# Kernel optimization log

Measured on AMD Instinct MI355X. Metric: run time of the kernel, lower is better.

Reference implementation:

```python
import jax, jax.numpy as jnp
import numpy as np

NEG_SLOPE = 0.01


def reference(feat_src, feat_dst, src, dst, attn_l, attn_r):
    # feat_src: [Ns, D], feat_dst: [Nd, D], src/dst: [E] int, attn_*: [1, D]
    n_dst = feat_dst.shape[0]
    el = (feat_src * attn_l).sum(axis=-1)  # [Ns]
    er = (feat_dst * attn_r).sum(axis=-1)  # [Nd]
    e = el[src] + er[dst]                  # [E]
    e = jnp.where(e >= 0, e, NEG_SLOPE * e)  # leaky_relu
    # edge softmax over incoming edges of each destination node
    m = jax.ops.segment_max(e, dst, num_segments=n_dst)  # [Nd]
    m = jnp.where(jnp.isfinite(m), m, 0.0)  # guard empty segments
    a = jnp.exp(e - m[dst])                 # [E]
    denom = jax.ops.segment_sum(a, dst, num_segments=n_dst)  # [Nd]
    denom = jnp.where(denom > 0, denom, 1.0)
    a = a / denom[dst]
    # weighted scatter-sum of source features: [E, D] messages -> [Nd, D]
    msg = feat_src[src] * a[:, None]
    out = jax.ops.segment_sum(msg, dst, num_segments=n_dst)
    return out


def setup_inputs() -> dict:
    key = jax.random.key(0)
    k1, k2, k3, k4, k5, k6 = jax.random.split(key, 6)
    Ns, Nd, E, D = 100000, 100000, 1600000, 128
    return {
        "feat_src": jax.random.normal(k1, (Ns, D), dtype=jnp.float32),
        "feat_dst": jax.random.normal(k2, (Nd, D), dtype=jnp.float32),
        "src": jax.random.randint(k3, (E,), 0, Ns, dtype=jnp.int32),
        "dst": jax.random.randint(k4, (E,), 0, Nd, dtype=jnp.int32),
        "attn_l": jax.random.normal(k5, (1, D), dtype=jnp.float32) * 0.1,
        "attn_r": jax.random.normal(k6, (1, D), dtype=jnp.float32) * 0.1,
    }
```

## Files before the change

### kernel.cpp

```cpp
#include <hip/hip_runtime.h>
#include <hip/hip_bf16.h>
#include <math.h>

#define D 128
#define AGG_THREADS 128
#define CHUNK 512
#define BSHIFT 8
#define MAXB 512
#define MAXWG 1024
#define PCHUNK 2048
#define PE 8
#define EBUF_CAP 5120
#define PR 8192

__device__ __forceinline__ unsigned short f2bf(float f) {
    union { float f; unsigned int u; } c; c.f = f;
    unsigned int u = c.u;
    unsigned int r = (u + 0x7FFFu + ((u >> 16) & 1u)) >> 16;
    return (unsigned short)r;
}
__device__ __forceinline__ void unpack2(unsigned int w, float& lo, float& hi) {
    union { unsigned int u; float f; } c;
    c.u = w << 16;          lo = c.f;
    c.u = w & 0xFFFF0000u;  hi = c.f;
}

__device__ __forceinline__ int scan8w(const int* __restrict__ arr, int* __restrict__ outp,
                                      int n, int tid, int* wsum8) {
    int wv = tid >> 6, lane = tid & 63;
    int nchunk = (n + 63) >> 6;
    int cpw = (nchunk + 7) >> 3;
    int c0 = wv * cpw, c1 = min(nchunk, c0 + cpw);
    int carry = 0;
    for (int c = c0; c < c1; ++c) {
        int i = (c << 6) + lane;
        int v = (i < n) ? arr[i] : 0;
        int x = v;
        #pragma unroll
        for (int off = 1; off < 64; off <<= 1) {
            int t = __shfl_up(x, off, 64);
            if (lane >= off) x += t;
        }
        if (i < n) outp[i] = x - v + carry;
        carry += __shfl(x, 63, 64);
    }
    if (lane == 0) wsum8[wv] = carry;
    __syncthreads();
    int wbase = 0;
    for (int u = 0; u < wv; ++u) wbase += wsum8[u];
    if (wbase) {
        for (int c = c0; c < c1; ++c) {
            int i = (c << 6) + lane;
            if (i < n) outp[i] += wbase;
        }
    }
    int tot = 0;
    #pragma unroll
    for (int u = 0; u < 8; ++u) tot += wsum8[u];
    __syncthreads();
    return tot;
}

__global__ void prep_partition_kernel(const float* __restrict__ feat_src,
                                      const float* __restrict__ feat_dst,
                                      const float* __restrict__ attn_l,
                                      const float* __restrict__ attn_r,
                                      float* __restrict__ el, float* __restrict__ er,
                                      unsigned short* __restrict__ feat_bf,
                                      int Ns, int Nd,
                                      const int* __restrict__ src,
                                      const int* __restrict__ dst,
                                      int E, int nbk, int nwg,
                                      uint2* __restrict__ bins,
                                      int* __restrict__ cnt_tab,
                                      int* __restrict__ loc_tab) {
    __shared__ int hist[MAXB];
    __shared__ int lstart[MAXB];
    __shared__ int cursor[MAXB];
    __shared__ uint2 sbuf[PCHUNK];
    int tid = threadIdx.x;

    if ((int)blockIdx.x < nwg) {
        int w = blockIdx.x;
        int e0 = w * PCHUNK;
        int e1 = min(E, e0 + PCHUNK);
        int n = e1 - e0;

        for (int i = tid; i < nbk; i += 256) hist[i] = 0;
        __syncthreads();

        int es[PE], ed[PE];
        #pragma unroll
        for (int k = 0; k < PE; ++k) {
            int idx = e0 + k * 256 + tid;
            if (idx < e1) {
                es[k] = src[idx];
                ed[k] = dst[idx];
                atomicAdd(&hist[ed[k] >> BSHIFT], 1);
            }
        }
        __syncthreads();

        if (tid < 64) {
            int carry = 0;
            for (int c = 0; c < nbk; c += 64) {
                int i = c + tid;
                int v = (i < nbk) ? hist[i] : 0;
                int x = v;
                #pragma unroll
                for (int off = 1; off < 64; off <<= 1) {
                    int t = __shfl_up(x, off, 64);
                    if (tid >= off) x += t;
                }
                if (i < nbk) lstart[i] = x - v + carry;
                carry += __shfl(x, 63, 64);
            }
        }
        __syncthreads();

        for (int i = tid; i < nbk; i += 256) {
            cnt_tab[(size_t)w * nbk + i] = hist[i];
            loc_tab[(size_t)w * nbk + i] = lstart[i];
            cursor[i] = 0;
        }
        __syncthreads();

        #pragma unroll
        for (int k = 0; k < PE; ++k) {
            int idx = e0 + k * 256 + tid;
            if (idx < e1) {
                int b = ed[k] >> BSHIFT;
                int r = lstart[b] + atomicAdd(&cursor[b], 1);
                sbuf[r] = make_uint2((unsigned)es[k], (unsigned)ed[k]);
            }
        }
        __syncthreads();

        uint2* obase = bins + (size_t)w * PCHUNK;
        for (int t = tid; t < n; t += 256) obase[t] = sbuf[t];
    } else {
        int half = tid >> 5;
        int lane = tid & 31;
        int node = ((int)blockIdx.x - nwg) * 8 + half;
        if (node >= Ns + Nd) return;
        bool is_src = node < Ns;
        const float* feat = is_src ? feat_src + (size_t)node * D
                                   : feat_dst + (size_t)(node - Ns) * D;
        const float* attn = is_src ? attn_l : attn_r;
        float4 a = ((const float4*)attn)[lane];
        float4 v = ((const float4*)feat)[lane];
        if (is_src) {
            ushort4 h; h.x = f2bf(v.x); h.y = f2bf(v.y); h.z = f2bf(v.z); h.w = f2bf(v.w);
            ((ushort4*)(feat_bf + (size_t)node * D))[lane] = h;
        }
        float s = v.x * a.x + v.y * a.y + v.z * a.z + v.w * a.w;
        #pragma unroll
        for (int off = 16; off > 0; off >>= 1)
            s += __shfl_xor(s, off, 64);
        if (lane == 0) {
            if (is_src) el[node] = s;
            else        er[node - Ns] = s;
        }
    }
}

__global__ void prep_kernel(const float* __restrict__ feat_src,
                            const float* __restrict__ feat_dst,
                            const float* __restrict__ attn_l,
                            const float* __restrict__ attn_r,
                            float* __restrict__ el, float* __restrict__ er,
                            unsigned short* __restrict__ feat_bf, int store_bf,
                            int Ns, int Nd) {
    int half = threadIdx.x >> 5;
    int lane = threadIdx.x & 31;
    int node = blockIdx.x * 8 + half;
    if (node >= Ns + Nd) return;
    bool is_src = node < Ns;
    const float* feat = is_src ? feat_src + (size_t)node * D
                               : feat_dst + (size_t)(node - Ns) * D;
    const float* attn = is_src ? attn_l : attn_r;
    float4 a = ((const float4*)attn)[lane];
    float4 v = ((const float4*)feat)[lane];
    if (is_src && store_bf) {
        ushort4 h; h.x = f2bf(v.x); h.y = f2bf(v.y); h.z = f2bf(v.z); h.w = f2bf(v.w);
        ((ushort4*)(feat_bf + (size_t)node * D))[lane] = h;
    }
    float s = v.x * a.x + v.y * a.y + v.z * a.z + v.w * a.w;
    #pragma unroll
    for (int off = 16; off > 0; off >>= 1)
        s += __shfl_xor(s, off, 64);
    if (lane == 0) {
        if (is_src) el[node] = s;
        else        er[node - Ns] = s;
    }
}

__global__ void bucket_kernel(const uint2* __restrict__ bins,
                              const int* __restrict__ cnt_tab, const int* __restrict__ loc_tab,
                              int nbk, int nwg,
                              int* __restrict__ counts, int* __restrict__ offs,
                              int* __restrict__ perm, int Nd) {
    __shared__ uint2 ebuf[EBUF_CAP];
    __shared__ int wcnt[MAXWG];
    __shared__ int wdst[MAXWG];
    __shared__ int sbase[MAXWG];
    __shared__ int cnt256[256];
    __shared__ int off256[256];
    __shared__ int cur256[256];
    __shared__ int wsum8[8];

    int b = blockIdx.x, tid = threadIdx.x;
    int base = b << BSHIFT;

    for (int i = tid; i < nwg; i += 512) wcnt[i] = cnt_tab[(size_t)i * nbk + b];
    if (tid < 256) { cnt256[tid] = 0; cur256[tid] = 0; }
    __syncthreads();

    int n = scan8w(wcnt, wdst, nwg, tid, wsum8);
    bool fits = (n <= EBUF_CAP);

    for (int w = tid; w < nwg; w += 512)
        sbase[w] = w * PCHUNK + loc_tab[(size_t)w * nbk + b] - wdst[w];
    __syncthreads();

    if (fits) {
        for (int w = tid; w < nwg; w += 512) {
            int c = wcnt[w];
            if (c) {
                const uint2* sp = bins + (size_t)(sbase[w] + wdst[w]);
                int d0 = wdst[w];
                for (int k = 0; k < c; ++k) {
                    uint2 e = sp[k];
                    ebuf[d0 + k] = e;
                    atomicAdd(&cnt256[(int)e.y - base], 1);
                }
            }
        }
    } else {
        for (int w = tid; w < nwg; w += 512) {
            int c = wcnt[w];
            const uint2* sp = bins + (size_t)(sbase[w] + wdst[w]);
            for (int k = 0; k < c; ++k)
                atomicAdd(&cnt256[(int)sp[k].y - base], 1);
        }
    }
    __syncthreads();

    scan8w(cnt256, off256, 256, tid, wsum8);
    if (tid < 256) {
        int v = cnt256[tid];
        int myoff = off256[tid];
        int i = base + tid;
        if (i < Nd) {
            int c = v;
            if (myoff + c > PR) c = max(0, PR - myoff);
            counts[i] = c;
            offs[i]   = myoff;
        }
    }
    __syncthreads();

    size_t rbase = (size_t)b * PR;
    if (fits) {
        for (int t = tid; t < n; t += 512) {
            uint2 e = ebuf[t];
            int d = (int)e.y - base;
            int r = atomicAdd(&cur256[d], 1);
            int slot = off256[d] + r;
            if (slot < PR) perm[rbase + slot] = (int)e.x;
        }
    } else {
        for (int w = tid; w < nwg; w += 512) {
            int c = wcnt[w];
            const uint2* sp = bins + (size_t)(sbase[w] + wdst[w]);
            for (int k = 0; k < c; ++k) {
                uint2 e = sp[k];
                int d = (int)e.y - base;
                int r = atomicAdd(&cur256[d], 1);
                int slot = off256[d] + r;
                if (slot < PR) perm[rbase + slot] = (int)e.x;
            }
        }
    }
}

__device__ __forceinline__ float block_max128(float v, float* red, int tid) {
    #pragma unroll
    for (int off = 32; off > 0; off >>= 1)
        v = fmaxf(v, __shfl_down(v, off, 64));
    __syncthreads();
    if ((tid & 63) == 0) red[tid >> 6] = v;
    __syncthreads();
    return fmaxf(red[0], red[1]);
}
__device__ __forceinline__ float block_sum128(float v, float* red, int tid) {
    #pragma unroll
    for (int off = 32; off > 0; off >>= 1)
        v += __shfl_down(v, off, 64);
    __syncthreads();
    if ((tid & 63) == 0) red[tid >> 6] = v;
    __syncthreads();
    return red[0] + red[1];
}

__global__ void gat_aggregate_wave_kernel(const unsigned short* __restrict__ feat_bf,
                                          const float* __restrict__ el,
                                          const float* __restrict__ er,
                                          const int* __restrict__ offs,
                                          const int* __restrict__ counts,
                                          const int* __restrict__ perm,
                                          float* __restrict__ out, int Nd) {
    int wid  = threadIdx.x >> 6;
    int lane = threadIdx.x & 63;
    int j = blockIdx.x * 4 + wid;
    if (j >= Nd) return;
    int cnt = counts[j];
    size_t orow = (size_t)j * D;
    if (cnt == 0) {
        ((float2*)(out + orow))[lane] = make_float2(0.0f, 0.0f);
        return;
    }
    size_t beg = (size_t)(j >> BSHIFT) * PR + (size_t)offs[j];
    float erj = er[j];
    int sg = lane >> 4, u = lane & 15;
    const unsigned short* fb = feat_bf + (size_t)u * 8;
    float acc[8];
    #pragma unroll
    for (int k = 0; k < 8; ++k) acc[k] = 0.0f;

    if (cnt <= 64) {
        int s = 0; float e = -INFINITY;
        if (lane < cnt) {
            s = perm[beg + lane];
            float t = el[s] + erj;
            e = (t >= 0.0f) ? t : 0.01f * t;
        }
        float m = e;
        #pragma unroll
        for (int off = 32; off > 0; off >>= 1)
            m = fmaxf(m, __shfl_xor(m, off, 64));
        float a = (lane < cnt) ? __expf(e - m) : 0.0f;
        float den = a;
        #pragma unroll
        for (int off = 32; off > 0; off >>= 1)
            den += __shfl_xor(den, off, 64);
        a *= (1.0f / den);
        int nit = (cnt + 3) >> 2;
        int it = 0;
        for (; it + 4 <= nit; it += 4) {
            int t0 = sg + (it << 2);
            int t1 = t0 + 4;
            int t2 = t0 + 8;
            int t3 = t0 + 12;
            int u1 = (t1 < cnt) ? t1 : 0;
            int u2 = (t2 < cnt) ? t2 : 0;
            int u3 = (t3 < cnt) ? t3 : 0;
            float w0 = __shfl(a, t0, 64); int s0 = __shfl(s, t0, 64);
            float w1 = __shfl(a, u1, 64); int s1 = __shfl(s, u1, 64);
            float w2 = __shfl(a, u2, 64); int s2 = __shfl(s, u2, 64);
            float w3 = __shfl(a, u3, 64); int s3 = __shfl(s, u3, 64);
            bool p1 = (t1 < cnt), p2 = (t2 < cnt), p3 = (t3 < cnt);
            uint4 v0 = *(const uint4*)(fb + (size_t)s0 * D);
            uint4 v1 = p1 ? *(const uint4*)(fb + (size_t)s1 * D) : make_uint4(0,0,0,0);
            uint4 v2 = p2 ? *(const uint4*)(fb + (size_t)s2 * D) : make_uint4(0,0,0,0);
            uint4 v3 = p3 ? *(const uint4*)(fb + (size_t)s3 * D) : make_uint4(0,0,0,0);
            float f[8];
            unpack2(v0.x, f[0], f[1]); unpack2(v0.y, f[2], f[3]);
            unpack2(v0.z, f[4], f[5]); unpack2(v0.w, f[6], f[7]);
            #pragma unroll
            for (int k = 0; k < 8; ++k) acc[k] += w0 * f[k];
            if (p1) {
                unpack2(v1.x, f[0], f[1]); unpack2(v1.y, f[2], f[3]);
                unpack2(v1.z, f[4], f[5]); unpack2(v1.w, f[6], f[7]);
                #pragma unroll
                for (int k = 0; k < 8; ++k) acc[k] += w1 * f[k];
            }
            if (p2) {
                unpack2(v2.x, f[0], f[1]); unpack2(v2.y, f[2], f[3]);
                unpack2(v2.z, f[4], f[5]); unpack2(v2.w, f[6], f[7]);
                #pragma unroll
                for (int k = 0; k < 8; ++k) acc[k] += w2 * f[k];
            }
            if (p3) {
                unpack2(v3.x, f[0], f[1]); unpack2(v3.y, f[2], f[3]);
                unpack2(v3.z, f[4], f[5]); unpack2(v3.w, f[6], f[7]);
                #pragma unroll
                for (int k = 0; k < 8; ++k) acc[k] += w3 * f[k];
            }
        }
        for (; it < nit; ++it) {
            int t0 = sg + (it << 2);
            int u0 = (t0 < cnt) ? t0 : 0;
            float w0 = __shfl(a, u0, 64);
            int   s0 = __shfl(s, u0, 64);
            if (t0 < cnt) {
                uint4 v0 = *(const uint4*)(fb + (size_t)s0 * D);
                float f[8];
                unpack2(v0.x, f[0], f[1]); unpack2(v0.y, f[2], f[3]);
                unpack2(v0.z, f[4], f[5]); unpack2(v0.w, f[6], f[7]);
                #pragma unroll
                for (int k = 0; k < 8; ++k) acc[k] += w0 * f[k];
            }
        }
    } else {
        float lmax = -INFINITY;
        for (int t = lane; t < cnt; t += 64) {
            int s = perm[beg + t];
            float e = el[s] + erj;
            e = (e >= 0.0f) ? e : 0.01f * e;
            lmax = fmaxf(lmax, e);
        }
        float m = lmax;
        #pragma unroll
        for (int off = 32; off > 0; off >>= 1)
            m = fmaxf(m, __shfl_xor(m, off, 64));
        float lsum = 0.0f;
        for (int t = lane; t < cnt; t += 64) {
            int s = perm[beg + t];
            float e = el[s] + erj;
            e = (e >= 0.0f) ? e : 0.01f * e;
            lsum += __expf(e - m);
        }
        #pragma unroll
        for (int off = 32; off > 0; off >>= 1)
            lsum += __shfl_xor(lsum, off, 64);
        float inv = 1.0f / lsum;
        for (int bb = 0; bb < cnt; bb += 64) {
            int nn = min(64, cnt - bb);
            int s = 0; float a = 0.0f;
            if (lane < nn) {
                s = perm[beg + bb + lane];
                float e = el[s] + erj;
                e = (e >= 0.0f) ? e : 0.01f * e;
                a = __expf(e - m) * inv;
            }
            int nit = (nn + 3) >> 2;
            for (int it = 0; it < nit; ++it) {
                int t = sg + (it << 2);
                int tt = (t < nn) ? t : 0;
                float w = __shfl(a, tt, 64);
                int st  = __shfl(s, tt, 64);
                if (t < nn) {
                    uint4 v = *(const uint4*)(fb + (size_t)st * D);
                    float f[8];
                    unpack2(v.x, f[0], f[1]); unpack2(v.y, f[2], f[3]);
                    unpack2(v.z, f[4], f[5]); unpack2(v.w, f[6], f[7]);
                    #pragma unroll
                    for (int k = 0; k < 8; ++k) acc[k] += w * f[k];
                }
            }
        }
    }
    #pragma unroll
    for (int k = 0; k < 8; ++k) {
        acc[k] += __shfl_xor(acc[k], 16, 64);
        acc[k] += __shfl_xor(acc[k], 32, 64);
    }
    if (sg == 0) {
        float* op = out + orow + (size_t)u * 8;
        ((float4*)op)[0] = make_float4(acc[0], acc[1], acc[2], acc[3]);
        ((float4*)op)[1] = make_float4(acc[4], acc[5], acc[6], acc[7]);
    }
}

__global__ void hist_kernel(const int* __restrict__ dst, int E, int* __restrict__ counts) {
    int stride = gridDim.x * blockDim.x;
    for (int k = blockIdx.x * blockDim.x + threadIdx.x; k < E; k += stride)
        atomicAdd(&counts[dst[k]], 1);
}
__global__ void scan1_kernel(const int* __restrict__ counts, int* __restrict__ offsets,
                             int* __restrict__ blockSums, int N) {
    __shared__ int tile[256];
    int tid = threadIdx.x;
    int i = blockIdx.x * 256 + tid;
    int v = (i < N) ? counts[i] : 0;
    tile[tid] = v;
    __syncthreads();
    for (int off = 1; off < 256; off <<= 1) {
        int t = (tid >= off) ? tile[tid - off] : 0;
        __syncthreads();
        tile[tid] += t;
        __syncthreads();
    }
    int incl = tile[tid];
    if (i < N) offsets[i] = incl - v;
    if (tid == 255) blockSums[blockIdx.x] = incl;
}
__global__ void scan2_kernel(int* __restrict__ bs, int nb) {
    __shared__ int tile[256];
    int tid = threadIdx.x;
    int carry = 0;
    for (int base = 0; base < nb; base += 256) {
        int i = base + tid;
        int v = (i < nb) ? bs[i] : 0;
        __syncthreads();
        tile[tid] = v;
        __syncthreads();
        for (int off = 1; off < 256; off <<= 1) {
            int t = (tid >= off) ? tile[tid - off] : 0;
            __syncthreads();
            tile[tid] += t;
            __syncthreads();
        }
        int incl = tile[tid];
        if (i < nb) bs[i] = incl - v + carry;
        carry += tile[255];
    }
}
__global__ void fill_kernel(const int* __restrict__ src, const int* __restrict__ dst, int E,
                            const int* __restrict__ offsets, const int* __restrict__ bsum,
                            int* __restrict__ cursor, int* __restrict__ perm_src) {
    int stride = gridDim.x * blockDim.x;
    for (int k = blockIdx.x * blockDim.x + threadIdx.x; k < E; k += stride) {
        int j = dst[k];
        int p = offsets[j] + bsum[j >> BSHIFT] + atomicAdd(&cursor[j], 1);
        perm_src[p] = src[k];
    }
}
__global__ void gat_aggregate_f32_kernel(const float* __restrict__ feat_src,
                                         const float* __restrict__ el,
                                         const float* __restrict__ er,
                                         const int* __restrict__ offsets,
                                         const int* __restrict__ bsum,
                                         const int* __restrict__ counts,
                                         const int* __restrict__ perm_src,
                                         float* __restrict__ out, int Nd) {
    __shared__ float w_sh[CHUNK];
    __shared__ int   s_sh[CHUNK];
    __shared__ float red[2];
    int j = blockIdx.x;
    int tid = threadIdx.x;
    int cnt = counts[j];
    size_t orow = (size_t)j * D;
    if (cnt == 0) { out[orow + tid] = 0.0f; return; }
    int beg = offsets[j] + bsum[j >> BSHIFT];
    float erj = er[j];
    float acc = 0.0f;
    float inv;
    if (cnt <= CHUNK) {
        float lmax = -INFINITY;
        for (int t = tid; t < cnt; t += AGG_THREADS) {
            int s = perm_src[beg + t];
            float e = el[s] + erj;
            e = (e >= 0.0f) ? e : 0.01f * e;
            s_sh[t] = s; w_sh[t] = e;
            lmax = fmaxf(lmax, e);
        }
        float m = block_max128(lmax, red, tid);
        float lsum = 0.0f;
        for (int t = tid; t < cnt; t += AGG_THREADS) {
            float a = __expf(w_sh[t] - m);
            w_sh[t] = a; lsum += a;
        }
        float den = block_sum128(lsum, red, tid);
        inv = 1.0f / den;
        __syncthreads();
        for (int t = 0; t < cnt; ++t)
            acc += feat_src[(size_t)s_sh[t] * D + tid] * w_sh[t];
    } else {
        float lmax = -INFINITY;
        for (int t = tid; t < cnt; t += AGG_THREADS) {
            int s = perm_src[beg + t];
            float e = el[s] + erj;
            e = (e >= 0.0f) ? e : 0.01f * e;
            lmax = fmaxf(lmax, e);
        }
        float m = block_max128(lmax, red, tid);
        float lsum = 0.0f;
        for (int t = tid; t < cnt; t += AGG_THREADS) {
            int s = perm_src[beg + t];
            float e = el[s] + erj;
            e = (e >= 0.0f) ? e : 0.01f * e;
            lsum += __expf(e - m);
        }
        float den = block_sum128(lsum, red, tid);
        inv = 1.0f / den;
        for (int bb = 0; bb < cnt; bb += CHUNK) {
            int n = min(CHUNK, cnt - bb);
            __syncthreads();
            for (int t = tid; t < n; t += AGG_THREADS) {
                int s = perm_src[beg + bb + t];
                float e = el[s] + erj;
                e = (e >= 0.0f) ? e : 0.01f * e;
                s_sh[t] = s;
                w_sh[t] = __expf(e - m);
            }
            __syncthreads();
            for (int t = 0; t < n; ++t)
                acc += feat_src[(size_t)s_sh[t] * D + tid] * w_sh[t];
        }
    }
    out[orow + tid] = acc * inv;
}

extern "C" void kernel_launch(void* const* d_in, const int* in_sizes, int n_in,
                              void* d_out, int out_size, void* d_ws, size_t ws_size,
                              hipStream_t stream) {
    const float* feat_src = (const float*)d_in[0];
    const float* feat_dst = (const float*)d_in[1];
    const int*   src      = (const int*)d_in[2];
    const int*   dst      = (const int*)d_in[3];
    const float* attn_l   = (const float*)d_in[4];
    const float* attn_r   = (const float*)d_in[5];
    float* out = (float*)d_out;

    int Ns = in_sizes[0] / D;
    int Nd = in_sizes[1] / D;
    int E  = in_sizes[2];
    int NBK = (Nd + (1 << BSHIFT) - 1) >> BSHIFT;
    int NWG = (E + PCHUNK - 1) / PCHUNK;

    char* p = (char*)d_ws;
    auto carve = [&](size_t bytes) { void* r = (void*)p; p += (bytes + 255) & ~(size_t)255; return r; };
    float* el      = (float*)carve((size_t)Ns * 4);
    float* er      = (float*)carve((size_t)Nd * 4);
    int*   counts  = (int*)carve((size_t)Nd * 4);
    int*   offs    = (int*)carve((size_t)Nd * 4);
    int*   gcursor = (int*)carve((size_t)Nd * 4);
    int*   bsums   = (int*)carve((size_t)NBK * 4);
    int*   cnt_tab = (int*)carve((size_t)NWG * NBK * 4);
    int*   loc_tab = (int*)carve((size_t)NWG * NBK * 4);
    int*   perm    = (int*)carve((size_t)NBK * PR * 4);
    uint2* bins    = (uint2*)carve((size_t)NWG * PCHUNK * 8);
    size_t used    = (size_t)(p - (char*)d_ws);
    size_t bf_bytes = (size_t)Ns * D * 2;
    unsigned short* feat_bf = (unsigned short*)carve(bf_bytes);

    int fast = (NBK <= MAXB && NWG <= MAXWG &&
                used + bf_bytes + 256 <= ws_size) ? 1 : 0;

    int total = Ns + Nd;
    int prep_blocks = (total + 7) / 8;
    if (fast) {
        prep_partition_kernel<<<NWG + prep_blocks, 256, 0, stream>>>(
            feat_src, feat_dst, attn_l, attn_r, el, er, feat_bf, Ns, Nd,
            src, dst, E, NBK, NWG, bins, cnt_tab, loc_tab);
        bucket_kernel<<<NBK, 512, 0, stream>>>(bins, cnt_tab, loc_tab, NBK, NWG,
                                               counts, offs, perm, Nd);
        gat_aggregate_wave_kernel<<<(Nd + 3) / 4, 256, 0, stream>>>(feat_bf, el, er, offs,
                                                                    counts, perm, out, Nd);
    } else {
        hipMemsetAsync(counts, 0, (size_t)Nd * 4, stream);
        hipMemsetAsync(gcursor, 0, (size_t)Nd * 4, stream);
        prep_kernel<<<prep_blocks, 256, 0, stream>>>(feat_src, feat_dst, attn_l, attn_r,
                                                     el, er, nullptr, 0, Ns, Nd);
        hist_kernel<<<2048, 256, 0, stream>>>(dst, E, counts);
        scan1_kernel<<<NBK, 256, 0, stream>>>(counts, offs, bsums, Nd);
        scan2_kernel<<<1, 256, 0, stream>>>(bsums, NBK);
        fill_kernel<<<2048, 256, 0, stream>>>(src, dst, E, offs, bsums, gcursor, perm);
        gat_aggregate_f32_kernel<<<Nd, AGG_THREADS, 0, stream>>>(feat_src, el, er, offs,
                                                                 bsums, counts, perm, out, Nd);
    }
}
```

Baseline: 243.6 us.

## Process two destination nodes per wavefront using half-waves for small degrees

Each wavefront now handles two destination nodes, with each 32-lane half-wave doing softmax and aggregation for one node when both degrees are at most 32. If either node has a larger degree, the wave falls back to processing the two nodes one after another with the full wave. This targets idle lanes in the softmax stage, since average degree is about 16, and halves the number of launched waves. In exchange, each half-wave has fewer edges in flight per iteration, and a mixed pair pays the serial fallback cost.

```diff
diff --git a/kernel.cpp b/kernel.cpp
--- a/kernel.cpp
+++ b/kernel.cpp
@@ -312,87 +312,78 @@
                                           float* __restrict__ out, int Nd) {
     int wid  = threadIdx.x >> 6;
     int lane = threadIdx.x & 63;
-    int j = blockIdx.x * 4 + wid;
-    if (j >= Nd) return;
-    int cnt = counts[j];
-    size_t orow = (size_t)j * D;
-    if (cnt == 0) {
-        ((float2*)(out + orow))[lane] = make_float2(0.0f, 0.0f);
-        return;
-    }
-    size_t beg = (size_t)(j >> BSHIFT) * PR + (size_t)offs[j];
-    float erj = er[j];
-    int sg = lane >> 4, u = lane & 15;
-    const unsigned short* fb = feat_bf + (size_t)u * 8;
-    float acc[8];
+    int jbase = blockIdx.x * 8 + wid * 2;
+    if (jbase >= Nd) return;
+
+    int halfid = lane >> 5;
+    int hl = lane & 31;
+    int j = jbase + halfid;
+    bool jv = (j < Nd);
+    int cnt = jv ? counts[j] : 0;
+
+    int mc = cnt;
     #pragma unroll
-    for (int k = 0; k < 8; ++k) acc[k] = 0.0f;
-
-    if (cnt <= 64) {
+    for (int off = 32; off > 0; off >>= 1)
+        mc = max(mc, __shfl_xor(mc, off, 64));
+
+    if (mc <= 32) {
+        size_t beg = jv ? ((size_t)(j >> BSHIFT) * PR + (size_t)offs[j]) : 0;
+        float erj = jv ? er[j] : 0.0f;
         int s = 0; float e = -INFINITY;
-        if (lane < cnt) {
-            s = perm[beg + lane];
+        if (hl < cnt) {
+            s = perm[beg + hl];
             float t = el[s] + erj;
             e = (t >= 0.0f) ? t : 0.01f * t;
         }
         float m = e;
         #pragma unroll
-        for (int off = 32; off > 0; off >>= 1)
+        for (int off = 16; off > 0; off >>= 1)
             m = fmaxf(m, __shfl_xor(m, off, 64));
-        float a = (lane < cnt) ? __expf(e - m) : 0.0f;
+        float a = (hl < cnt) ? __expf(e - m) : 0.0f;
         float den = a;
         #pragma unroll
-        for (int off = 32; off > 0; off >>= 1)
+        for (int off = 16; off > 0; off >>= 1)
             den += __shfl_xor(den, off, 64);
-        a *= (1.0f / den);
-        int nit = (cnt + 3) >> 2;
+        a *= (den > 0.0f) ? (1.0f / den) : 0.0f;
+
+        int sg2 = hl >> 4, u = hl & 15;
+        const unsigned short* fb = feat_bf + (size_t)u * 8;
+        int hbase = halfid << 5;
+        float acc[8];
+        #pragma unroll
+        for (int k = 0; k < 8; ++k) acc[k] = 0.0f;
+
+        int nit = (mc + 1) >> 1;
         int it = 0;
-        for (; it + 4 <= nit; it += 4) {
-            int t0 = sg + (it << 2);
-            int t1 = t0 + 4;
-            int t2 = t0 + 8;
-            int t3 = t0 + 12;
+        for (; it + 2 <= nit; it += 2) {
+            int t0 = sg2 + (it << 1);
+            int t1 = t0 + 2;
+            int u0 = (t0 < cnt) ? t0 : 0;
             int u1 = (t1 < cnt) ? t1 : 0;
-            int u2 = (t2 < cnt) ? t2 : 0;
-            int u3 = (t3 < cnt) ? t3 : 0;
-            float w0 = __shfl(a, t0, 64); int s0 = __shfl(s, t0, 64);
-            float w1 = __shfl(a, u1, 64); int s1 = __shfl(s, u1, 64);
-            float w2 = __shfl(a, u2, 64); int s2 = __shfl(s, u2, 64);
-            float w3 = __shfl(a, u3, 64); int s3 = __shfl(s, u3, 64);
-            bool p1 = (t1 < cnt), p2 = (t2 < cnt), p3 = (t3 < cnt);
-            uint4 v0 = *(const uint4*)(fb + (size_t)s0 * D);
+            float w0 = __shfl(a, hbase + u0, 64); int s0 = __shfl(s, hbase + u0, 64);
+            float w1 = __shfl(a, hbase + u1, 64); int s1 = __shfl(s, hbase + u1, 64);
+            bool p0 = (t0 < cnt), p1 = (t1 < cnt);
+            uint4 v0 = p0 ? *(const uint4*)(fb + (size_t)s0 * D) : make_uint4(0,0,0,0);
             uint4 v1 = p1 ? *(const uint4*)(fb + (size_t)s1 * D) : make_uint4(0,0,0,0);
-            uint4 v2 = p2 ? *(const uint4*)(fb + (size_t)s2 * D) : make_uint4(0,0,0,0);
-            uint4 v3 = p3 ? *(const uint4*)(fb + (size_t)s3 * D) : make_uint4(0,0,0,0);
             float f[8];
-            unpack2(v0.x, f[0], f[1]); unpack2(v0.y, f[2], f[3]);
-            unpack2(v0.z, f[4], f[5]); unpack2(v0.w, f[6], f[7]);
-            #pragma unroll
-            for (int k = 0; k < 8; ++k) acc[k] += w0 * f[k];
+            if (p0) {
+                unpack2(v0.x, f[0], f[1]); unpack2(v0.y, f[2], f[3]);
+                unpack2(v0.z, f[4], f[5]); unpack2(v0.w, f[6], f[7]);
+                #pragma unroll
+                for (int k = 0; k < 8; ++k) acc[k] += w0 * f[k];
+            }
             if (p1) {
                 unpack2(v1.x, f[0], f[1]); unpack2(v1.y, f[2], f[3]);
                 unpack2(v1.z, f[4], f[5]); unpack2(v1.w, f[6], f[7]);
                 #pragma unroll
                 for (int k = 0; k < 8; ++k) acc[k] += w1 * f[k];
             }
-            if (p2) {
-                unpack2(v2.x, f[0], f[1]); unpack2(v2.y, f[2], f[3]);
-                unpack2(v2.z, f[4], f[5]); unpack2(v2.w, f[6], f[7]);
-                #pragma unroll
-                for (int k = 0; k < 8; ++k) acc[k] += w2 * f[k];
-            }
-            if (p3) {
-                unpack2(v3.x, f[0], f[1]); unpack2(v3.y, f[2], f[3]);
-                unpack2(v3.z, f[4], f[5]); unpack2(v3.w, f[6], f[7]);
-                #pragma unroll
-                for (int k = 0; k < 8; ++k) acc[k] += w3 * f[k];
-            }
-        }
-        for (; it < nit; ++it) {
-            int t0 = sg + (it << 2);
+        }
+        if (it < nit) {
+            int t0 = sg2 + (it << 1);
             int u0 = (t0 < cnt) ? t0 : 0;
-            float w0 = __shfl(a, u0, 64);
-            int   s0 = __shfl(s, u0, 64);
+            float w0 = __shfl(a, hbase + u0, 64);
+            int   s0 = __shfl(s, hbase + u0, 64);
             if (t0 < cnt) {
                 uint4 v0 = *(const uint4*)(fb + (size_t)s0 * D);
                 float f[8];
@@ -402,45 +393,58 @@
                 for (int k = 0; k < 8; ++k) acc[k] += w0 * f[k];
             }
         }
-    } else {
-        float lmax = -INFINITY;
-        for (int t = lane; t < cnt; t += 64) {
-            int s = perm[beg + t];
-            float e = el[s] + erj;
-            e = (e >= 0.0f) ? e : 0.01f * e;
-            lmax = fmaxf(lmax, e);
-        }
-        float m = lmax;
-        #pragma unroll
-        for (int off = 32; off > 0; off >>= 1)
-            m = fmaxf(m, __shfl_xor(m, off, 64));
-        float lsum = 0.0f;
-        for (int t = lane; t < cnt; t += 64) {
-            int s = perm[beg + t];
-            float e = el[s] + erj;
-            e = (e >= 0.0f) ? e : 0.01f * e;
-            lsum += __expf(e - m);
-        }
-        #pragma unroll
-        for (int off = 32; off > 0; off >>= 1)
-            lsum += __shfl_xor(lsum, off, 64);
-        float inv = 1.0f / lsum;
-        for (int bb = 0; bb < cnt; bb += 64) {
-            int nn = min(64, cnt - bb);
-            int s = 0; float a = 0.0f;
-            if (lane < nn) {
-                s = perm[beg + bb + lane];
-                float e = el[s] + erj;
-                e = (e >= 0.0f) ? e : 0.01f * e;
-                a = __expf(e - m) * inv;
-            }
-            int nit = (nn + 3) >> 2;
+        #pragma unroll
+        for (int k = 0; k < 8; ++k)
+            acc[k] += __shfl_xor(acc[k], 16, 64);
+        if (sg2 == 0 && jv) {
+            float* op = out + (size_t)j * D + (size_t)u * 8;
+            ((float4*)op)[0] = make_float4(acc[0], acc[1], acc[2], acc[3]);
+            ((float4*)op)[1] = make_float4(acc[4], acc[5], acc[6], acc[7]);
+        }
+        return;
+    }
+
+    int sg = lane >> 4, u = lane & 15;
+    const unsigned short* fb = feat_bf + (size_t)u * 8;
+    for (int q = 0; q < 2; ++q) {
+        int jj = jbase + q;
+        if (jj >= Nd) break;
+        int cq = counts[jj];
+        size_t orow = (size_t)jj * D;
+        if (cq == 0) {
+            ((float2*)(out + orow))[lane] = make_float2(0.0f, 0.0f);
+            continue;
+        }
+        size_t beg = (size_t)(jj >> BSHIFT) * PR + (size_t)offs[jj];
+        float erj = er[jj];
+        float acc[8];
+        #pragma unroll
+        for (int k = 0; k < 8; ++k) acc[k] = 0.0f;
+
+        if (cq <= 64) {
+            int s = 0; float e = -INFINITY;
+            if (lane < cq) {
+                s = perm[beg + lane];
+                float t = el[s] + erj;
+                e = (t >= 0.0f) ? t : 0.01f * t;
+            }
+            float m = e;
+            #pragma unroll
+            for (int off = 32; off > 0; off >>= 1)
+                m = fmaxf(m, __shfl_xor(m, off, 64));
+            float a = (lane < cq) ? __expf(e - m) : 0.0f;
+            float den = a;
+            #pragma unroll
+            for (int off = 32; off > 0; off >>= 1)
+                den += __shfl_xor(den, off, 64);
+            a *= (1.0f / den);
+            int nit = (cq + 3) >> 2;
             for (int it = 0; it < nit; ++it) {
                 int t = sg + (it << 2);
-                int tt = (t < nn) ? t : 0;
+                int tt = (t < cq) ? t : 0;
                 float w = __shfl(a, tt, 64);
                 int st  = __shfl(s, tt, 64);
-                if (t < nn) {
+                if (t < cq) {
                     uint4 v = *(const uint4*)(fb + (size_t)st * D);
                     float f[8];
                     unpack2(v.x, f[0], f[1]); unpack2(v.y, f[2], f[3]);
@@ -449,17 +453,65 @@
                     for (int k = 0; k < 8; ++k) acc[k] += w * f[k];
                 }
             }
-        }
-    }
-    #pragma unroll
-    for (int k = 0; k < 8; ++k) {
-        acc[k] += __shfl_xor(acc[k], 16, 64);
-        acc[k] += __shfl_xor(acc[k], 32, 64);
-    }
-    if (sg == 0) {
-        float* op = out + orow + (size_t)u * 8;
-        ((float4*)op)[0] = make_float4(acc[0], acc[1], acc[2], acc[3]);
-        ((float4*)op)[1] = make_float4(acc[4], acc[5], acc[6], acc[7]);
+        } else {
+            float lmax = -INFINITY;
+            for (int t = lane; t < cq; t += 64) {
+                int s = perm[beg + t];
+                float e = el[s] + erj;
+                e = (e >= 0.0f) ? e : 0.01f * e;
+                lmax = fmaxf(lmax, e);
+            }
+            float m = lmax;
+            #pragma unroll
+            for (int off = 32; off > 0; off >>= 1)
+                m = fmaxf(m, __shfl_xor(m, off, 64));
+            float lsum = 0.0f;
+            for (int t = lane; t < cq; t += 64) {
+                int s = perm[beg + t];
+                float e = el[s] + erj;
+                e = (e >= 0.0f) ? e : 0.01f * e;
+                lsum += __expf(e - m);
+            }
+            #pragma unroll
+            for (int off = 32; off > 0; off >>= 1)
+                lsum += __shfl_xor(lsum, off, 64);
+            float inv = 1.0f / lsum;
+            for (int bb = 0; bb < cq; bb += 64) {
+                int nn = min(64, cq - bb);
+                int s = 0; float a = 0.0f;
+                if (lane < nn) {
+                    s = perm[beg + bb + lane];
+                    float e = el[s] + erj;
+                    e = (e >= 0.0f) ? e : 0.01f * e;
+                    a = __expf(e - m) * inv;
+                }
+                int nit = (nn + 3) >> 2;
+                for (int it = 0; it < nit; ++it) {
+                    int t = sg + (it << 2);
+                    int tt = (t < nn) ? t : 0;
+                    float w = __shfl(a, tt, 64);
+                    int st  = __shfl(s, tt, 64);
+                    if (t < nn) {
+                        uint4 v = *(const uint4*)(fb + (size_t)st * D);
+                        float f[8];
+                        unpack2(v.x, f[0], f[1]); unpack2(v.y, f[2], f[3]);
+                        unpack2(v.z, f[4], f[5]); unpack2(v.w, f[6], f[7]);
+                        #pragma unroll
+                        for (int k = 0; k < 8; ++k) acc[k] += w * f[k];
+                    }
+                }
+            }
+        }
+        #pragma unroll
+        for (int k = 0; k < 8; ++k) {
+            acc[k] += __shfl_xor(acc[k], 16, 64);
+            acc[k] += __shfl_xor(acc[k], 32, 64);
+        }
+        if (sg == 0) {
+            float* op = out + orow + (size_t)u * 8;
+            ((float4*)op)[0] = make_float4(acc[0], acc[1], acc[2], acc[3]);
+            ((float4*)op)[1] = make_float4(acc[4], acc[5], acc[6], acc[7]);
+        }
     }
 }
 
@@ -637,7 +689,7 @@
             src, dst, E, NBK, NWG, bins, cnt_tab, loc_tab);
         bucket_kernel<<<NBK, 512, 0, stream>>>(bins, cnt_tab, loc_tab, NBK, NWG,
                                                counts, offs, perm, Nd);
-        gat_aggregate_wave_kernel<<<(Nd + 3) / 4, 256, 0, stream>>>(feat_bf, el, er, offs,
+        gat_aggregate_wave_kernel<<<(Nd + 7) / 8, 256, 0, stream>>>(feat_bf, el, er, offs,
                                                                     counts, perm, out, Nd);
     } else {
         hipMemsetAsync(counts, 0, (size_t)Nd * 4, stream);
```

Result: no change. 240.9 us, median of 2 (-1.1%).
